# Performance work log

Measured on AMD Instinct MI355X. Metric: run time of the kernel, lower is better.

## Reference

```python
import jax, jax.numpy as jnp
import numpy as np

DIM = 4096
LOG_DIM = int(np.log2(DIM))  # 12
BATCH = 8192


def setup_inputs() -> dict:
    key = jax.random.key(0)
    k1, k2, k3 = jax.random.split(key, 3)
    x = jax.random.normal(k1, (BATCH, DIM), dtype=jnp.float32)
    # packed per-layer rotation params: layer l has DIM >> (l+1) blocks;
    # total = DIM - 1 = 4095. Original init: a=cos(theta), b=sin(theta), theta~0.01*N(0,1)
    theta = jax.random.normal(k2, (DIM - 1,), dtype=jnp.float32) * 0.01
    a_flat = jnp.cos(theta)
    b_flat = jnp.sin(theta)
    del k3
    return {"x": x, "a_flat": a_flat, "b_flat": b_flat}


def reference(x, a_flat, b_flat):
    B, D = x.shape
    off = 0
    for layer in range(LOG_DIM):
        bs = 1 << layer                  # block_size = 2**layer
        nb = D // (2 * bs)               # num_blocks
        a = a_flat[off:off + nb][None, :, None]  # [1, nb, 1]
        b = b_flat[off:off + nb][None, :, None]
        off += nb
        xv = x.reshape(B, nb, 2, bs)
        x0 = xv[:, :, 0, :]
        x1 = xv[:, :, 1, :]
        top = a * x0 + b * x1
        bot = -b * x0 + a * x1
        x = jnp.stack([top, bot], axis=2).reshape(B, D)
    return x
```

## Files before the change

### kernel.cpp

```cpp
#include <hip/hip_runtime.h>

#define DIM   4096
#define BATCH 8192

__device__ __forceinline__ void rot2(float& lo, float& hi, float a, float b) {
    float l = lo, h = hi;
    lo = fmaf(a, l,  b * h);
    hi = fmaf(a, h, -b * l);
}

template<bool PACKED>
__device__ __forceinline__ float2 coef(const float* __restrict__ af,
                                       const float* __restrict__ bf,
                                       const float2* __restrict__ ab, int c) {
    if constexpr (PACKED) return ab[c];
    else                  return make_float2(af[c], bf[c]);
}

template<int M, int JSH, int LSH, bool PACKED>
__device__ __forceinline__ void shuf_layer(float4* v, int lane, int base,
                                           const float* __restrict__ af,
                                           const float* __restrict__ bf,
                                           const float2* __restrict__ ab) {
    #pragma unroll
    for (int j = 0; j < 4; ++j) {
        const int c = base + (j << JSH) + (lane >> LSH);
        float2 q = coef<PACKED>(af, bf, ab, c);
        const float sb = (lane & M) ? -q.y : q.y;
        v[j].x = fmaf(q.x, v[j].x, sb * __shfl_xor(v[j].x, M, 64));
        v[j].y = fmaf(q.x, v[j].y, sb * __shfl_xor(v[j].y, M, 64));
        v[j].z = fmaf(q.x, v[j].z, sb * __shfl_xor(v[j].z, M, 64));
        v[j].w = fmaf(q.x, v[j].w, sb * __shfl_xor(v[j].w, M, 64));
    }
}

template<bool PACKED>
__global__ __launch_bounds__(256, 8)
void bfly_kernel(const float* __restrict__ x,
                 const float* __restrict__ af,
                 const float* __restrict__ bf,
                 const float2* __restrict__ ab,
                 float* __restrict__ out) {
    const int lane = threadIdx.x & 63;
    const int q    = threadIdx.x >> 6;
    const size_t row = blockIdx.x;

    const float4* __restrict__ xr = reinterpret_cast<const float4*>(x + row * DIM) + q * 256;
    float4* __restrict__ orow     = reinterpret_cast<float4*>(out + row * DIM) + q * 256;

    __shared__ float4 xch[4][4][64];

    float4 v[4];
    #pragma unroll
    for (int j = 0; j < 4; ++j) v[j] = xr[64 * j + lane];

    #pragma unroll
    for (int j = 0; j < 4; ++j) {
        float a0, b0, a1, b1;
        if constexpr (PACKED) {
            float4 p = reinterpret_cast<const float4*>(ab)[q * 256 + 64 * j + lane];
            a0 = p.x; b0 = p.y; a1 = p.z; b1 = p.w;
        } else {
            const int c = 512 * q + 128 * j + 2 * lane;
            float2 aa = *reinterpret_cast<const float2*>(af + c);
            float2 bb = *reinterpret_cast<const float2*>(bf + c);
            a0 = aa.x; b0 = bb.x; a1 = aa.y; b1 = bb.y;
        }
        rot2(v[j].x, v[j].y, a0, b0);
        rot2(v[j].z, v[j].w, a1, b1);
    }

    #pragma unroll
    for (int j = 0; j < 4; ++j) {
        float2 p = coef<PACKED>(af, bf, ab, 2048 + 256 * q + 64 * j + lane);
        rot2(v[j].x, v[j].z, p.x, p.y);
        rot2(v[j].y, v[j].w, p.x, p.y);
    }

    shuf_layer< 1, 5, 1, PACKED>(v, lane, 3072 + 128 * q, af, bf, ab);
    shuf_layer< 2, 4, 2, PACKED>(v, lane, 3584 +  64 * q, af, bf, ab);
    shuf_layer< 4, 3, 3, PACKED>(v, lane, 3840 +  32 * q, af, bf, ab);
    shuf_layer< 8, 2, 4, PACKED>(v, lane, 3968 +  16 * q, af, bf, ab);
    shuf_layer<16, 1, 5, PACKED>(v, lane, 4032 +   8 * q, af, bf, ab);
    shuf_layer<32, 0, 6, PACKED>(v, lane, 4064 +   4 * q, af, bf, ab);

    #pragma unroll
    for (int k = 0; k < 2; ++k) {
        float2 p = coef<PACKED>(af, bf, ab, 4080 + 2 * q + k);
        rot2(v[2*k].x, v[2*k+1].x, p.x, p.y);
        rot2(v[2*k].y, v[2*k+1].y, p.x, p.y);
        rot2(v[2*k].z, v[2*k+1].z, p.x, p.y);
        rot2(v[2*k].w, v[2*k+1].w, p.x, p.y);
    }
    {
        float2 p = coef<PACKED>(af, bf, ab, 4088 + q);
        #pragma unroll
        for (int j = 0; j < 2; ++j) {
            rot2(v[j].x, v[j+2].x, p.x, p.y);
            rot2(v[j].y, v[j+2].y, p.x, p.y);
            rot2(v[j].z, v[j+2].z, p.x, p.y);
            rot2(v[j].w, v[j+2].w, p.x, p.y);
        }
    }

    {
        float2 p = coef<PACKED>(af, bf, ab, 4092 + (q >> 1));
        const float sb = (q & 1) ? -p.y : p.y;
        #pragma unroll
        for (int j = 0; j < 4; ++j) xch[q][j][lane] = v[j];
        __syncthreads();
        #pragma unroll
        for (int j = 0; j < 4; ++j) {
            float4 w = xch[q ^ 1][j][lane];
            v[j].x = fmaf(p.x, v[j].x, sb * w.x);
            v[j].y = fmaf(p.x, v[j].y, sb * w.y);
            v[j].z = fmaf(p.x, v[j].z, sb * w.z);
            v[j].w = fmaf(p.x, v[j].w, sb * w.w);
        }
    }
    __syncthreads();
    {
        float2 p = coef<PACKED>(af, bf, ab, 4094);
        const float sb = (q & 2) ? -p.y : p.y;
        #pragma unroll
        for (int j = 0; j < 4; ++j) xch[q][j][lane] = v[j];
        __syncthreads();
        #pragma unroll
        for (int j = 0; j < 4; ++j) {
            float4 w = xch[q ^ 2][j][lane];
            v[j].x = fmaf(p.x, v[j].x, sb * w.x);
            v[j].y = fmaf(p.x, v[j].y, sb * w.y);
            v[j].z = fmaf(p.x, v[j].z, sb * w.z);
            v[j].w = fmaf(p.x, v[j].w, sb * w.w);
        }
    }

    #pragma unroll
    for (int j = 0; j < 4; ++j) orow[64 * j + lane] = v[j];
}

__global__ void pack_ab_kernel(const float* __restrict__ af,
                               const float* __restrict__ bf,
                               float2* __restrict__ ab) {
    int i = blockIdx.x * 256 + threadIdx.x;
    if (i < DIM - 1) ab[i] = make_float2(af[i], bf[i]);
}

extern "C" void kernel_launch(void* const* d_in, const int* in_sizes, int n_in,
                              void* d_out, int out_size, void* d_ws, size_t ws_size,
                              hipStream_t stream) {
    const float* x  = (const float*)d_in[0];
    const float* af = (const float*)d_in[1];
    const float* bf = (const float*)d_in[2];
    float* out      = (float*)d_out;

    const bool packed = (d_ws != nullptr) && (ws_size >= (size_t)(DIM - 1) * sizeof(float2));
    if (packed) {
        float2* ab = (float2*)d_ws;
        hipLaunchKernelGGL(pack_ab_kernel, dim3(16), dim3(256), 0, stream, af, bf, ab);
        hipLaunchKernelGGL((bfly_kernel<true>),  dim3(BATCH), dim3(256), 0, stream,
                           x, af, bf, ab, out);
    } else {
        hipLaunchKernelGGL((bfly_kernel<false>), dim3(BATCH), dim3(256), 0, stream,
                           x, af, bf, nullptr, out);
    }
}
```

Baseline: 58.65 us.

## Process two rows per block and merge final two cross-wave layers

```diff
diff --git a/kernel.cpp b/kernel.cpp
--- a/kernel.cpp
+++ b/kernel.cpp
@@ -18,7 +18,7 @@
 }
 
 template<int M, int JSH, int LSH, bool PACKED>
-__device__ __forceinline__ void shuf_layer(float4* v, int lane, int base,
+__device__ __forceinline__ void shuf_layer(float4 (&v)[2][4], int lane, int base,
                                            const float* __restrict__ af,
                                            const float* __restrict__ bf,
                                            const float2* __restrict__ ab) {
@@ -27,15 +27,18 @@
         const int c = base + (j << JSH) + (lane >> LSH);
         float2 q = coef<PACKED>(af, bf, ab, c);
         const float sb = (lane & M) ? -q.y : q.y;
-        v[j].x = fmaf(q.x, v[j].x, sb * __shfl_xor(v[j].x, M, 64));
-        v[j].y = fmaf(q.x, v[j].y, sb * __shfl_xor(v[j].y, M, 64));
-        v[j].z = fmaf(q.x, v[j].z, sb * __shfl_xor(v[j].z, M, 64));
-        v[j].w = fmaf(q.x, v[j].w, sb * __shfl_xor(v[j].w, M, 64));
+        #pragma unroll
+        for (int r = 0; r < 2; ++r) {
+            v[r][j].x = fmaf(q.x, v[r][j].x, sb * __shfl_xor(v[r][j].x, M, 64));
+            v[r][j].y = fmaf(q.x, v[r][j].y, sb * __shfl_xor(v[r][j].y, M, 64));
+            v[r][j].z = fmaf(q.x, v[r][j].z, sb * __shfl_xor(v[r][j].z, M, 64));
+            v[r][j].w = fmaf(q.x, v[r][j].w, sb * __shfl_xor(v[r][j].w, M, 64));
+        }
     }
 }
 
 template<bool PACKED>
-__global__ __launch_bounds__(256, 8)
+__global__ __launch_bounds__(256, 5)
 void bfly_kernel(const float* __restrict__ x,
                  const float* __restrict__ af,
                  const float* __restrict__ bf,
@@ -43,16 +46,23 @@
                  float* __restrict__ out) {
     const int lane = threadIdx.x & 63;
     const int q    = threadIdx.x >> 6;
-    const size_t row = blockIdx.x;
 
-    const float4* __restrict__ xr = reinterpret_cast<const float4*>(x + row * DIM) + q * 256;
-    float4* __restrict__ orow     = reinterpret_cast<float4*>(out + row * DIM) + q * 256;
+    const float4* __restrict__ xr0 =
+        reinterpret_cast<const float4*>(x + (size_t)(blockIdx.x * 2 + 0) * DIM) + q * 256;
+    const float4* __restrict__ xr1 =
+        reinterpret_cast<const float4*>(x + (size_t)(blockIdx.x * 2 + 1) * DIM) + q * 256;
+    float4* __restrict__ or0 =
+        reinterpret_cast<float4*>(out + (size_t)(blockIdx.x * 2 + 0) * DIM) + q * 256;
+    float4* __restrict__ or1 =
+        reinterpret_cast<float4*>(out + (size_t)(blockIdx.x * 2 + 1) * DIM) + q * 256;
 
-    __shared__ float4 xch[4][4][64];
+    __shared__ float4 xch[2][4][4][64];
 
-    float4 v[4];
+    float4 v[2][4];
     #pragma unroll
-    for (int j = 0; j < 4; ++j) v[j] = xr[64 * j + lane];
+    for (int j = 0; j < 4; ++j) v[0][j] = xr0[64 * j + lane];
+    #pragma unroll
+    for (int j = 0; j < 4; ++j) v[1][j] = xr1[64 * j + lane];
 
     #pragma unroll
     for (int j = 0; j < 4; ++j) {
@@ -66,15 +76,21 @@
             float2 bb = *reinterpret_cast<const float2*>(bf + c);
             a0 = aa.x; b0 = bb.x; a1 = aa.y; b1 = bb.y;
         }
-        rot2(v[j].x, v[j].y, a0, b0);
-        rot2(v[j].z, v[j].w, a1, b1);
+        #pragma unroll
+        for (int r = 0; r < 2; ++r) {
+            rot2(v[r][j].x, v[r][j].y, a0, b0);
+            rot2(v[r][j].z, v[r][j].w, a1, b1);
+        }
     }
 
     #pragma unroll
     for (int j = 0; j < 4; ++j) {
         float2 p = coef<PACKED>(af, bf, ab, 2048 + 256 * q + 64 * j + lane);
-        rot2(v[j].x, v[j].z, p.x, p.y);
-        rot2(v[j].y, v[j].w, p.x, p.y);
+        #pragma unroll
+        for (int r = 0; r < 2; ++r) {
+            rot2(v[r][j].x, v[r][j].z, p.x, p.y);
+            rot2(v[r][j].y, v[r][j].w, p.x, p.y);
+        }
     }
 
     shuf_layer< 1, 5, 1, PACKED>(v, lane, 3072 + 128 * q, af, bf, ab);
@@ -87,56 +103,66 @@
     #pragma unroll
     for (int k = 0; k < 2; ++k) {
         float2 p = coef<PACKED>(af, bf, ab, 4080 + 2 * q + k);
-        rot2(v[2*k].x, v[2*k+1].x, p.x, p.y);
-        rot2(v[2*k].y, v[2*k+1].y, p.x, p.y);
-        rot2(v[2*k].z, v[2*k+1].z, p.x, p.y);
-        rot2(v[2*k].w, v[2*k+1].w, p.x, p.y);
+        #pragma unroll
+        for (int r = 0; r < 2; ++r) {
+            rot2(v[r][2*k].x, v[r][2*k+1].x, p.x, p.y);
+            rot2(v[r][2*k].y, v[r][2*k+1].y, p.x, p.y);
+            rot2(v[r][2*k].z, v[r][2*k+1].z, p.x, p.y);
+            rot2(v[r][2*k].w, v[r][2*k+1].w, p.x, p.y);
+        }
     }
     {
         float2 p = coef<PACKED>(af, bf, ab, 4088 + q);
         #pragma unroll
-        for (int j = 0; j < 2; ++j) {
-            rot2(v[j].x, v[j+2].x, p.x, p.y);
-            rot2(v[j].y, v[j+2].y, p.x, p.y);
-            rot2(v[j].z, v[j+2].z, p.x, p.y);
-            rot2(v[j].w, v[j+2].w, p.x, p.y);
-        }
+        for (int r = 0; r < 2; ++r)
+            #pragma unroll
+            for (int j = 0; j < 2; ++j) {
+                rot2(v[r][j].x, v[r][j+2].x, p.x, p.y);
+                rot2(v[r][j].y, v[r][j+2].y, p.x, p.y);
+                rot2(v[r][j].z, v[r][j+2].z, p.x, p.y);
+                rot2(v[r][j].w, v[r][j+2].w, p.x, p.y);
+            }
     }
 
     {
-        float2 p = coef<PACKED>(af, bf, ab, 4092 + (q >> 1));
-        const float sb = (q & 1) ? -p.y : p.y;
+        float2 c0 = coef<PACKED>(af, bf, ab, 4092);
+        float2 c1 = coef<PACKED>(af, bf, ab, 4093);
+        float2 c2 = coef<PACKED>(af, bf, ab, 4094);
+        const int h11 = q >> 1, h10 = q & 1;
+        const float aO = h11 ? c1.x : c0.x, bO = h11 ? c1.y : c0.y;
+        const float aX = h11 ? c0.x : c1.x, bX = h11 ? c0.y : c1.y;
+        const float phX = h11 ? -c2.y : c2.y;
+        const float w0 = c2.x * aO;
+        const float w1 = c2.x * (h10 ? -bO : bO);
+        const float w2 = phX * aX;
+        const float w3 = phX * (h10 ? -bX : bX);
+        const int q1 = q ^ 1, q2 = q ^ 2, q3 = q ^ 3;
+
         #pragma unroll
-        for (int j = 0; j < 4; ++j) xch[q][j][lane] = v[j];
+        for (int r = 0; r < 2; ++r)
+            #pragma unroll
+            for (int j = 0; j < 4; ++j) xch[r][q][j][lane] = v[r][j];
         __syncthreads();
         #pragma unroll
-        for (int j = 0; j < 4; ++j) {
-            float4 w = xch[q ^ 1][j][lane];
-            v[j].x = fmaf(p.x, v[j].x, sb * w.x);
-            v[j].y = fmaf(p.x, v[j].y, sb * w.y);
-            v[j].z = fmaf(p.x, v[j].z, sb * w.z);
-            v[j].w = fmaf(p.x, v[j].w, sb * w.w);
-        }
-    }
-    __syncthreads();
-    {
-        float2 p = coef<PACKED>(af, bf, ab, 4094);
-        const float sb = (q & 2) ? -p.y : p.y;
-        #pragma unroll
-        for (int j = 0; j < 4; ++j) xch[q][j][lane] = v[j];
-        __syncthreads();
-        #pragma unroll
-        for (int j = 0; j < 4; ++j) {
-            float4 w = xch[q ^ 2][j][lane];
-            v[j].x = fmaf(p.x, v[j].x, sb * w.x);
-            v[j].y = fmaf(p.x, v[j].y, sb * w.y);
-            v[j].z = fmaf(p.x, v[j].z, sb * w.z);
-            v[j].w = fmaf(p.x, v[j].w, sb * w.w);
-        }
+        for (int r = 0; r < 2; ++r)
+            #pragma unroll
+            for (int j = 0; j < 4; ++j) {
+                float4 e1 = xch[r][q1][j][lane];
+                float4 e2 = xch[r][q2][j][lane];
+                float4 e3 = xch[r][q3][j][lane];
+                float4 a;
+                a.x = fmaf(w3, e3.x, fmaf(w2, e2.x, fmaf(w1, e1.x, w0 * v[r][j].x)));
+                a.y = fmaf(w3, e3.y, fmaf(w2, e2.y, fmaf(w1, e1.y, w0 * v[r][j].y)));
+                a.z = fmaf(w3, e3.z, fmaf(w2, e2.z, fmaf(w1, e1.z, w0 * v[r][j].z)));
+                a.w = fmaf(w3, e3.w, fmaf(w2, e2.w, fmaf(w1, e1.w, w0 * v[r][j].w)));
+                v[r][j] = a;
+            }
     }
 
     #pragma unroll
-    for (int j = 0; j < 4; ++j) orow[64 * j + lane] = v[j];
+    for (int j = 0; j < 4; ++j) or0[64 * j + lane] = v[0][j];
+    #pragma unroll
+    for (int j = 0; j < 4; ++j) or1[64 * j + lane] = v[1][j];
 }
 
 __global__ void pack_ab_kernel(const float* __restrict__ af,
@@ -158,10 +184,10 @@
     if (packed) {
         float2* ab = (float2*)d_ws;
         hipLaunchKernelGGL(pack_ab_kernel, dim3(16), dim3(256), 0, stream, af, bf, ab);
-        hipLaunchKernelGGL((bfly_kernel<true>),  dim3(BATCH), dim3(256), 0, stream,
+        hipLaunchKernelGGL((bfly_kernel<true>),  dim3(BATCH / 2), dim3(256), 0, stream,
                            x, af, bf, ab, out);
     } else {
-        hipLaunchKernelGGL((bfly_kernel<false>), dim3(BATCH), dim3(256), 0, stream,
+        hipLaunchKernelGGL((bfly_kernel<false>), dim3(BATCH / 2), dim3(256), 0, stream,
                            x, af, bf, nullptr, out);
     }
 }
```

Result: slower. 182.7 us (+211.6%).

## Use DPP/swizzle/permlane for butterflies and merge last two LDS exchanges

Applied to the files above, without the earlier changes.

```diff
diff --git a/kernel.cpp b/kernel.cpp
--- a/kernel.cpp
+++ b/kernel.cpp
@@ -2,6 +2,15 @@
 
 #define DIM   4096
 #define BATCH 8192
+
+#if defined(__has_builtin)
+#  if __has_builtin(__builtin_amdgcn_permlane32_swap)
+#    define HAVE_PL32 1
+#  endif
+#endif
+#ifndef HAVE_PL32
+#  define HAVE_PL32 0
+#endif
 
 __device__ __forceinline__ void rot2(float& lo, float& hi, float a, float b) {
     float l = lo, h = hi;
@@ -17,25 +26,50 @@
     else                  return make_float2(af[c], bf[c]);
 }
 
+template<int M>
+__device__ __forceinline__ float pxor(float x, bool hi) {
+    int xi = __float_as_int(x);
+    if constexpr (M == 1)
+        return __int_as_float(__builtin_amdgcn_update_dpp(0, xi, 0xB1, 0xF, 0xF, true));
+    else if constexpr (M == 2)
+        return __int_as_float(__builtin_amdgcn_update_dpp(0, xi, 0x4E, 0xF, 0xF, true));
+    else if constexpr (M == 4)
+        return __int_as_float(__builtin_amdgcn_ds_swizzle(xi, 0x101F));
+    else if constexpr (M == 8)
+        return __int_as_float(__builtin_amdgcn_update_dpp(0, xi, 0x128, 0xF, 0xF, true));
+    else if constexpr (M == 16)
+        return __int_as_float(__builtin_amdgcn_ds_swizzle(xi, 0x401F));
+    else {
+#if HAVE_PL32
+        unsigned xu = (unsigned)xi;
+        auto r = __builtin_amdgcn_permlane32_swap(xu, xu, false, false);
+        return __uint_as_float(hi ? r[0] : r[1]);
+#else
+        return __shfl_xor(x, 32, 64);
+#endif
+    }
+}
+
 template<int M, int JSH, int LSH, bool PACKED>
-__device__ __forceinline__ void shuf_layer(float4* v, int lane, int base,
+__device__ __forceinline__ void shuf_layer(float4 (&v)[4], int lane, int base,
                                            const float* __restrict__ af,
                                            const float* __restrict__ bf,
                                            const float2* __restrict__ ab) {
+    const bool hi = (lane & M) != 0;
     #pragma unroll
     for (int j = 0; j < 4; ++j) {
         const int c = base + (j << JSH) + (lane >> LSH);
-        float2 q = coef<PACKED>(af, bf, ab, c);
-        const float sb = (lane & M) ? -q.y : q.y;
-        v[j].x = fmaf(q.x, v[j].x, sb * __shfl_xor(v[j].x, M, 64));
-        v[j].y = fmaf(q.x, v[j].y, sb * __shfl_xor(v[j].y, M, 64));
-        v[j].z = fmaf(q.x, v[j].z, sb * __shfl_xor(v[j].z, M, 64));
-        v[j].w = fmaf(q.x, v[j].w, sb * __shfl_xor(v[j].w, M, 64));
+        float2 p = coef<PACKED>(af, bf, ab, c);
+        const float sb = hi ? -p.y : p.y;
+        v[j].x = fmaf(p.x, v[j].x, sb * pxor<M>(v[j].x, hi));
+        v[j].y = fmaf(p.x, v[j].y, sb * pxor<M>(v[j].y, hi));
+        v[j].z = fmaf(p.x, v[j].z, sb * pxor<M>(v[j].z, hi));
+        v[j].w = fmaf(p.x, v[j].w, sb * pxor<M>(v[j].w, hi));
     }
 }
 
 template<bool PACKED>
-__global__ __launch_bounds__(256, 8)
+__global__ __launch_bounds__(256, 7)
 void bfly_kernel(const float* __restrict__ x,
                  const float* __restrict__ af,
                  const float* __restrict__ bf,
@@ -104,34 +138,33 @@
     }
 
     {
-        float2 p = coef<PACKED>(af, bf, ab, 4092 + (q >> 1));
-        const float sb = (q & 1) ? -p.y : p.y;
+        float2 c0 = coef<PACKED>(af, bf, ab, 4092);
+        float2 c1 = coef<PACKED>(af, bf, ab, 4093);
+        float2 c2 = coef<PACKED>(af, bf, ab, 4094);
+        const int h11 = q >> 1, h10 = q & 1;
+        const float aO = h11 ? c1.x : c0.x, bO = h11 ? c1.y : c0.y;
+        const float aX = h11 ? c0.x : c1.x, bX = h11 ? c0.y : c1.y;
+        const float phX = h11 ? -c2.y : c2.y;
+        const float w0 = c2.x * aO;
+        const float w1 = c2.x * (h10 ? -bO : bO);
+        const float w2 = phX * aX;
+        const float w3 = phX * (h10 ? -bX : bX);
+        const int q1 = q ^ 1, q2 = q ^ 2, q3 = q ^ 3;
+
         #pragma unroll
         for (int j = 0; j < 4; ++j) xch[q][j][lane] = v[j];
         __syncthreads();
         #pragma unroll
         for (int j = 0; j < 4; ++j) {
-            float4 w = xch[q ^ 1][j][lane];
-            v[j].x = fmaf(p.x, v[j].x, sb * w.x);
-            v[j].y = fmaf(p.x, v[j].y, sb * w.y);
-            v[j].z = fmaf(p.x, v[j].z, sb * w.z);
-            v[j].w = fmaf(p.x, v[j].w, sb * w.w);
-        }
-    }
-    __syncthreads();
-    {
-        float2 p = coef<PACKED>(af, bf, ab, 4094);
-        const float sb = (q & 2) ? -p.y : p.y;
-        #pragma unroll
-        for (int j = 0; j < 4; ++j) xch[q][j][lane] = v[j];
-        __syncthreads();
-        #pragma unroll
-        for (int j = 0; j < 4; ++j) {
-            float4 w = xch[q ^ 2][j][lane];
-            v[j].x = fmaf(p.x, v[j].x, sb * w.x);
-            v[j].y = fmaf(p.x, v[j].y, sb * w.y);
-            v[j].z = fmaf(p.x, v[j].z, sb * w.z);
-            v[j].w = fmaf(p.x, v[j].w, sb * w.w);
+            float4 e1 = xch[q1][j][lane];
+            float4 e2 = xch[q2][j][lane];
+            float4 e3 = xch[q3][j][lane];
+            float4 a;
+            a.x = fmaf(w3, e3.x, fmaf(w2, e2.x, fmaf(w1, e1.x, w0 * v[j].x)));
+            a.y = fmaf(w3, e3.y, fmaf(w2, e2.y, fmaf(w1, e1.y, w0 * v[j].y)));
+            a.z = fmaf(w3, e3.z, fmaf(w2, e2.z, fmaf(w1, e1.z, w0 * v[j].z)));
+            a.w = fmaf(w3, e3.w, fmaf(w2, e2.w, fmaf(w1, e1.w, w0 * v[j].w)));
+            v[j] = a;
         }
     }
 
```

Measured after the change: 56.42 us. -3.8%, faster.
